# Performance work log

Hardware: AMD Instinct MI355X
Metric: run time of the kernel (lower is better)

Reference implementation:

```python
import jax, jax.numpy as jnp
import numpy as np

EPS = 1e-5

def setup_inputs() -> dict:
    key = jax.random.key(0)
    ks = jax.random.split(key, 16)
    B, C, H, W, HID = 32, 512, 56, 56, 128
    inp = {
        "x": jax.random.normal(ks[0], (B, C, H, W), jnp.float32),
        "mod": jax.random.randint(ks[1], (B,), 0, 2, jnp.int32),
        "w1_rgb": jax.random.normal(ks[2], (HID, C), jnp.float32) * 0.05,
        "rm_rgb": jax.random.normal(ks[3], (HID,), jnp.float32) * 0.1,
        "rv_rgb": jax.random.uniform(ks[4], (HID,), jnp.float32, 0.5, 1.5),
        "g_rgb": jax.random.uniform(ks[5], (HID,), jnp.float32, 0.5, 1.5),
        "b_rgb": jax.random.normal(ks[6], (HID,), jnp.float32) * 0.1,
        "w2_rgb": jax.random.normal(ks[7], (C, HID), jnp.float32) * 0.05,
        "w1_inf": jax.random.normal(ks[8], (HID, C), jnp.float32) * 0.05,
        "rm_inf": jax.random.normal(ks[9], (HID,), jnp.float32) * 0.1,
        "rv_inf": jax.random.uniform(ks[10], (HID,), jnp.float32, 0.5, 1.5),
        "g_inf": jax.random.uniform(ks[11], (HID,), jnp.float32, 0.5, 1.5),
        "b_inf": jax.random.normal(ks[12], (HID,), jnp.float32) * 0.1,
        "w2_inf": jax.random.normal(ks[13], (C, HID), jnp.float32) * 0.05,
    }
    return inp

def _branch(x, w1, rm, rv, g, b, w2):
    # 1x1 conv (no bias) -> BN (inference, running stats) -> ReLU -> 1x1 conv
    h = jnp.einsum('bchw,oc->bohw', x, w1)              # (B,HID,H,W)
    scale = g / jnp.sqrt(rv + EPS)                       # (HID,)
    shift = b - rm * scale
    h = jax.nn.relu(h * scale[None, :, None, None] + shift[None, :, None, None])
    return jnp.einsum('bchw,oc->bohw', h, w2)            # (B,C,H,W)

def reference(x, mod, w1_rgb, rm_rgb, rv_rgb, g_rgb, b_rgb, w2_rgb,
              w1_inf, rm_inf, rv_inf, g_inf, b_inf, w2_inf):
    rgb = _branch(x, w1_rgb, rm_rgb, rv_rgb, g_rgb, b_rgb, w2_rgb)
    inf = _branch(x, w1_inf, rm_inf, rv_inf, g_inf, b_inf, w2_inf)
    is_rgb = (mod == 1)[:, None, None, None]
    out = jnp.where(is_rgb, rgb, inf)  # mod in {0,1}; dropout is identity (eval)
    return out
```

## Files before the change

### kernel.cpp

```cpp
#include <hip/hip_runtime.h>
#include <hip/hip_bf16.h>
#include <stdint.h>

#define B_   32
#define C_   512
#define HW_  3136
#define HID_ 128
#define PT   64
#define XP   72
#define HP   136
#define EPS_ 1e-5f

using frag8  = __attribute__((ext_vector_type(8))) short;
using short8 = __attribute__((ext_vector_type(8))) short;
using f32x4  = __attribute__((ext_vector_type(4))) float;

__device__ __forceinline__ short f2bf(float f) {
    union { float f; uint32_t u; } v; v.f = f;
    uint32_t u = v.u;
    u += 0x7fffu + ((u >> 16) & 1u);
    return (short)(u >> 16);
}

__global__ __launch_bounds__(256) void prep_kernel(
    const float* __restrict__ w1_rgb, const float* __restrict__ w2_rgb,
    const float* __restrict__ w1_inf, const float* __restrict__ w2_inf,
    const float* __restrict__ rm_rgb, const float* __restrict__ rv_rgb,
    const float* __restrict__ g_rgb,  const float* __restrict__ b_rgb,
    const float* __restrict__ rm_inf, const float* __restrict__ rv_inf,
    const float* __restrict__ g_inf,  const float* __restrict__ b_inf,
    short* __restrict__ w1p_rgb, short* __restrict__ w1p_inf,
    short* __restrict__ w2p_rgb, short* __restrict__ w2p_inf,
    float* __restrict__ ss)
{
    int t = blockIdx.x * 256 + threadIdx.x;
    int p = t >> 9, w = t & 511;
    int q = w >> 7, r = (w >> 3) & 15, j = w & 7;
    {
        int mt = p >> 4, kt = p & 15;
        int m = mt * 16 + r, k = kt * 32 + q * 8 + j;
        w1p_rgb[t] = f2bf(w1_rgb[m * C_ + k]);
        w1p_inf[t] = f2bf(w1_inf[m * C_ + k]);
    }
    {
        int mt = p >> 2, kt = p & 3;
        int m = mt * 16 + r, k = kt * 32 + q * 8 + j;
        w2p_rgb[t] = f2bf(w2_rgb[m * HID_ + k]);
        w2p_inf[t] = f2bf(w2_inf[m * HID_ + k]);
    }
    if (t < 128) {
        float sc = g_rgb[t] * rsqrtf(rv_rgb[t] + EPS_);
        ss[t] = sc; ss[128 + t] = b_rgb[t] - rm_rgb[t] * sc;
    } else if (t < 256) {
        int i = t - 128;
        float sc = g_inf[i] * rsqrtf(rv_inf[i] + EPS_);
        ss[256 + i] = sc; ss[384 + i] = b_inf[i] - rm_inf[i] * sc;
    }
}

__global__ __launch_bounds__(256) void fused_kernel(
    const float* __restrict__ x, const int* __restrict__ mod,
    const short* __restrict__ w1p_rgb, const short* __restrict__ w1p_inf,
    const short* __restrict__ w2p_rgb, const short* __restrict__ w2p_inf,
    const float* __restrict__ ss, float* __restrict__ out)
{
    __shared__ short xlds[2][PT * XP];
    __shared__ short hlds[PT * HP];

    const int tid  = threadIdx.x;
    const int lane = tid & 63;
    const int wave = tid >> 6;
    const int i16  = lane & 15;
    const int q    = lane >> 4;
    const int b    = blockIdx.y;
    const int p0   = blockIdx.x * PT;

    const int is_rgb = (mod[b] == 1);
    const short* __restrict__ w1p = is_rgb ? w1p_rgb : w1p_inf;
    const short* __restrict__ w2p = is_rgb ? w2p_rgb : w2p_inf;
    const float* __restrict__ scale = ss + (is_rgb ? 0 : 256);
    const float* __restrict__ shift = scale + 128;

    f32x4 acc1[2][4];
    #pragma unroll
    for (int mt = 0; mt < 2; ++mt)
        #pragma unroll
        for (int nt = 0; nt < 4; ++nt)
            acc1[mt][nt] = (f32x4){0.f, 0.f, 0.f, 0.f};

    const int px    = lane;
    const int cbase = wave * 8;
    const float* __restrict__ xb = x + (size_t)b * C_ * HW_ + p0 + px;

    float rA[16], rB[16];
    #pragma unroll
    for (int it = 0; it < 2; ++it)
        #pragma unroll
        for (int j = 0; j < 8; ++j)
            rA[it * 8 + j] = xb[(size_t)(cbase + it * 32 + j) * HW_];

    #pragma unroll 1
    for (int k2 = 0; k2 < 4; ++k2) {
        const int kcA = k2 * 2, kcB = kcA + 1;

        #pragma unroll
        for (int it = 0; it < 2; ++it) {
            short8 pk;
            #pragma unroll
            for (int j = 0; j < 8; ++j) pk[j] = f2bf(rA[it * 8 + j]);
            *(short8*)(&xlds[0][px * XP + cbase + it * 32]) = pk;
        }
        __syncthreads();

        #pragma unroll
        for (int it = 0; it < 2; ++it)
            #pragma unroll
            for (int j = 0; j < 8; ++j)
                rB[it * 8 + j] = xb[(size_t)(kcB * 64 + cbase + it * 32 + j) * HW_];

        {
            frag8 af[2][2];
            #pragma unroll
            for (int kk = 0; kk < 2; ++kk) {
                int kt = kcA * 2 + kk;
                #pragma unroll
                for (int mt = 0; mt < 2; ++mt)
                    af[kk][mt] = *(const frag8*)(w1p + (((wave * 2 + mt) * 16 + kt) << 9) + lane * 8);
            }
            #pragma unroll
            for (int kk = 0; kk < 2; ++kk) {
                frag8 bfr[4];
                #pragma unroll
                for (int nt = 0; nt < 4; ++nt)
                    bfr[nt] = *(const frag8*)(&xlds[0][(nt * 16 + i16) * XP + kk * 32 + q * 8]);
                #pragma unroll
                for (int mt = 0; mt < 2; ++mt)
                    #pragma unroll
                    for (int nt = 0; nt < 4; ++nt)
                        acc1[mt][nt] = __builtin_amdgcn_mfma_f32_16x16x32_bf16(
                            af[kk][mt], bfr[nt], acc1[mt][nt], 0, 0, 0);
            }
        }

        #pragma unroll
        for (int it = 0; it < 2; ++it) {
            short8 pk;
            #pragma unroll
            for (int j = 0; j < 8; ++j) pk[j] = f2bf(rB[it * 8 + j]);
            *(short8*)(&xlds[1][px * XP + cbase + it * 32]) = pk;
        }
        __syncthreads();

        if (k2 < 3) {
            #pragma unroll
            for (int it = 0; it < 2; ++it)
                #pragma unroll
                for (int j = 0; j < 8; ++j)
                    rA[it * 8 + j] = xb[(size_t)((kcA + 2) * 64 + cbase + it * 32 + j) * HW_];
        }

        {
            frag8 af[2][2];
            #pragma unroll
            for (int kk = 0; kk < 2; ++kk) {
                int kt = kcB * 2 + kk;
                #pragma unroll
                for (int mt = 0; mt < 2; ++mt)
                    af[kk][mt] = *(const frag8*)(w1p + (((wave * 2 + mt) * 16 + kt) << 9) + lane * 8);
            }
            #pragma unroll
            for (int kk = 0; kk < 2; ++kk) {
                frag8 bfr[4];
                #pragma unroll
                for (int nt = 0; nt < 4; ++nt)
                    bfr[nt] = *(const frag8*)(&xlds[1][(nt * 16 + i16) * XP + kk * 32 + q * 8]);
                #pragma unroll
                for (int mt = 0; mt < 2; ++mt)
                    #pragma unroll
                    for (int nt = 0; nt < 4; ++nt)
                        acc1[mt][nt] = __builtin_amdgcn_mfma_f32_16x16x32_bf16(
                            af[kk][mt], bfr[nt], acc1[mt][nt], 0, 0, 0);
            }
        }
    }

    #pragma unroll
    for (int mt = 0; mt < 2; ++mt) {
        int mbase = wave * 32 + mt * 16 + q * 4;
        float s0 = scale[mbase + 0], s1 = scale[mbase + 1];
        float s2 = scale[mbase + 2], s3 = scale[mbase + 3];
        float h0 = shift[mbase + 0], h1 = shift[mbase + 1];
        float h2 = shift[mbase + 2], h3 = shift[mbase + 3];
        #pragma unroll
        for (int nt = 0; nt < 4; ++nt) {
            int p = nt * 16 + i16;
            short4 pk = make_short4(
                f2bf(fmaxf(acc1[mt][nt][0] * s0 + h0, 0.f)),
                f2bf(fmaxf(acc1[mt][nt][1] * s1 + h1, 0.f)),
                f2bf(fmaxf(acc1[mt][nt][2] * s2 + h2, 0.f)),
                f2bf(fmaxf(acc1[mt][nt][3] * s3 + h3, 0.f)));
            *(short4*)(&hlds[p * HP + mbase]) = pk;
        }
    }
    __syncthreads();

    #pragma unroll 1
    for (int half = 0; half < 2; ++half) {
        f32x4 acc2[4][4];
        #pragma unroll
        for (int pt = 0; pt < 4; ++pt)
            #pragma unroll
            for (int ct = 0; ct < 4; ++ct)
                acc2[pt][ct] = (f32x4){0.f, 0.f, 0.f, 0.f};

        #pragma unroll
        for (int kt = 0; kt < 4; ++kt) {
            frag8 wf[4];
            #pragma unroll
            for (int ct = 0; ct < 4; ++ct) {
                int ctg = half * 16 + wave * 4 + ct;
                wf[ct] = *(const frag8*)(w2p + ((ctg * 4 + kt) << 9) + lane * 8);
            }
            frag8 hf[4];
            #pragma unroll
            for (int pt = 0; pt < 4; ++pt)
                hf[pt] = *(const frag8*)(&hlds[(pt * 16 + i16) * HP + kt * 32 + q * 8]);
            #pragma unroll
            for (int pt = 0; pt < 4; ++pt)
                #pragma unroll
                for (int ct = 0; ct < 4; ++ct)
                    acc2[pt][ct] = __builtin_amdgcn_mfma_f32_16x16x32_bf16(
                        hf[pt], wf[ct], acc2[pt][ct], 0, 0, 0);
        }
        #pragma unroll
        for (int ct = 0; ct < 4; ++ct) {
            int crow = (half * 16 + wave * 4 + ct) * 16 + i16;
            float* obase = out + ((size_t)(b * C_ + crow)) * HW_ + p0 + q * 4;
            #pragma unroll
            for (int pt = 0; pt < 4; ++pt)
                __builtin_nontemporal_store(acc2[pt][ct], (f32x4*)(obase + pt * 16));
        }
    }
}

extern "C" void kernel_launch(void* const* d_in, const int* in_sizes, int n_in,
                              void* d_out, int out_size, void* d_ws, size_t ws_size,
                              hipStream_t stream) {
    const float* x      = (const float*)d_in[0];
    const int*   mod    = (const int*)d_in[1];
    const float* w1_rgb = (const float*)d_in[2];
    const float* rm_rgb = (const float*)d_in[3];
    const float* rv_rgb = (const float*)d_in[4];
    const float* g_rgb  = (const float*)d_in[5];
    const float* b_rgb  = (const float*)d_in[6];
    const float* w2_rgb = (const float*)d_in[7];
    const float* w1_inf = (const float*)d_in[8];
    const float* rm_inf = (const float*)d_in[9];
    const float* rv_inf = (const float*)d_in[10];
    const float* g_inf  = (const float*)d_in[11];
    const float* b_inf  = (const float*)d_in[12];
    const float* w2_inf = (const float*)d_in[13];
    float* out = (float*)d_out;

    char* ws = (char*)d_ws;
    short* w1p_rgb = (short*)(ws + 0);
    short* w1p_inf = (short*)(ws + 131072);
    short* w2p_rgb = (short*)(ws + 262144);
    short* w2p_inf = (short*)(ws + 393216);
    float* ss      = (float*)(ws + 524288);

    prep_kernel<<<256, 256, 0, stream>>>(
        w1_rgb, w2_rgb, w1_inf, w2_inf,
        rm_rgb, rv_rgb, g_rgb, b_rgb,
        rm_inf, rv_inf, g_inf, b_inf,
        w1p_rgb, w1p_inf, w2p_rgb, w2p_inf, ss);

    dim3 grid(HW_ / PT, B_);
    fused_kernel<<<grid, 256, 0, stream>>>(
        x, mod, w1p_rgb, w1p_inf, w2p_rgb, w2p_inf, ss, out);
}
```

Before: 419.4 us.

## Deepen x prefetch to two chunks ahead with triple register buffering

The first GEMM's K loop over 512 channels is fully unrolled into 8 chunks with a triple-buffered register array. Global loads for chunk c+2 are issued while chunk c is converted and multiplied, so two chunks are in flight instead of one. This is meant to hide more global-memory latency on the strided x reads, at the cost of more VGPRs and possibly lower occupancy. The output stores also change from nontemporal to ordinary stores.

```diff
diff --git a/kernel.cpp b/kernel.cpp
--- a/kernel.cpp
+++ b/kernel.cpp
@@ -92,95 +92,58 @@
     const int cbase = wave * 8;
     const float* __restrict__ xb = x + (size_t)b * C_ * HW_ + p0 + px;
 
-    float rA[16], rB[16];
-    #pragma unroll
-    for (int it = 0; it < 2; ++it)
-        #pragma unroll
-        for (int j = 0; j < 8; ++j)
-            rA[it * 8 + j] = xb[(size_t)(cbase + it * 32 + j) * HW_];
-
-    #pragma unroll 1
-    for (int k2 = 0; k2 < 4; ++k2) {
-        const int kcA = k2 * 2, kcB = kcA + 1;
+    float r[3][16];
+    #pragma unroll
+    for (int c0 = 0; c0 < 2; ++c0)
+        #pragma unroll
+        for (int it = 0; it < 2; ++it)
+            #pragma unroll
+            for (int j = 0; j < 8; ++j)
+                r[c0][it * 8 + j] =
+                    xb[(size_t)(c0 * 64 + cbase + it * 32 + j) * HW_];
+
+    #pragma unroll
+    for (int c = 0; c < 8; ++c) {
+        const int rb = c % 3, lb = c & 1;
 
         #pragma unroll
         for (int it = 0; it < 2; ++it) {
             short8 pk;
             #pragma unroll
-            for (int j = 0; j < 8; ++j) pk[j] = f2bf(rA[it * 8 + j]);
-            *(short8*)(&xlds[0][px * XP + cbase + it * 32]) = pk;
+            for (int j = 0; j < 8; ++j) pk[j] = f2bf(r[rb][it * 8 + j]);
+            *(short8*)(&xlds[lb][px * XP + cbase + it * 32]) = pk;
         }
         __syncthreads();
 
-        #pragma unroll
-        for (int it = 0; it < 2; ++it)
-            #pragma unroll
-            for (int j = 0; j < 8; ++j)
-                rB[it * 8 + j] = xb[(size_t)(kcB * 64 + cbase + it * 32 + j) * HW_];
-
-        {
-            frag8 af[2][2];
-            #pragma unroll
-            for (int kk = 0; kk < 2; ++kk) {
-                int kt = kcA * 2 + kk;
-                #pragma unroll
-                for (int mt = 0; mt < 2; ++mt)
-                    af[kk][mt] = *(const frag8*)(w1p + (((wave * 2 + mt) * 16 + kt) << 9) + lane * 8);
-            }
-            #pragma unroll
-            for (int kk = 0; kk < 2; ++kk) {
-                frag8 bfr[4];
-                #pragma unroll
-                for (int nt = 0; nt < 4; ++nt)
-                    bfr[nt] = *(const frag8*)(&xlds[0][(nt * 16 + i16) * XP + kk * 32 + q * 8]);
-                #pragma unroll
-                for (int mt = 0; mt < 2; ++mt)
-                    #pragma unroll
-                    for (int nt = 0; nt < 4; ++nt)
-                        acc1[mt][nt] = __builtin_amdgcn_mfma_f32_16x16x32_bf16(
-                            af[kk][mt], bfr[nt], acc1[mt][nt], 0, 0, 0);
-            }
-        }
-
-        #pragma unroll
-        for (int it = 0; it < 2; ++it) {
-            short8 pk;
-            #pragma unroll
-            for (int j = 0; j < 8; ++j) pk[j] = f2bf(rB[it * 8 + j]);
-            *(short8*)(&xlds[1][px * XP + cbase + it * 32]) = pk;
-        }
-        __syncthreads();
-
-        if (k2 < 3) {
+        if (c + 2 < 8) {
             #pragma unroll
             for (int it = 0; it < 2; ++it)
                 #pragma unroll
                 for (int j = 0; j < 8; ++j)
-                    rA[it * 8 + j] = xb[(size_t)((kcA + 2) * 64 + cbase + it * 32 + j) * HW_];
-        }
-
-        {
-            frag8 af[2][2];
-            #pragma unroll
-            for (int kk = 0; kk < 2; ++kk) {
-                int kt = kcB * 2 + kk;
-                #pragma unroll
-                for (int mt = 0; mt < 2; ++mt)
-                    af[kk][mt] = *(const frag8*)(w1p + (((wave * 2 + mt) * 16 + kt) << 9) + lane * 8);
-            }
-            #pragma unroll
-            for (int kk = 0; kk < 2; ++kk) {
-                frag8 bfr[4];
+                    r[(c + 2) % 3][it * 8 + j] =
+                        xb[(size_t)((c + 2) * 64 + cbase + it * 32 + j) * HW_];
+        }
+
+        frag8 af[2][2];
+        #pragma unroll
+        for (int kk = 0; kk < 2; ++kk) {
+            int kt = c * 2 + kk;
+            #pragma unroll
+            for (int mt = 0; mt < 2; ++mt)
+                af[kk][mt] = *(const frag8*)(w1p + (((wave * 2 + mt) * 16 + kt) << 9) + lane * 8);
+        }
+        #pragma unroll
+        for (int kk = 0; kk < 2; ++kk) {
+            frag8 bfr[4];
+            #pragma unroll
+            for (int nt = 0; nt < 4; ++nt)
+                bfr[nt] = *(const frag8*)(&xlds[lb][(nt * 16 + i16) * XP + kk * 32 + q * 8]);
+            #pragma unroll
+            for (int mt = 0; mt < 2; ++mt)
                 #pragma unroll
                 for (int nt = 0; nt < 4; ++nt)
-                    bfr[nt] = *(const frag8*)(&xlds[1][(nt * 16 + i16) * XP + kk * 32 + q * 8]);
-                #pragma unroll
-                for (int mt = 0; mt < 2; ++mt)
-                    #pragma unroll
-                    for (int nt = 0; nt < 4; ++nt)
-                        acc1[mt][nt] = __builtin_amdgcn_mfma_f32_16x16x32_bf16(
-                            af[kk][mt], bfr[nt], acc1[mt][nt], 0, 0, 0);
-            }
+                    acc1[mt][nt] = __builtin_amdgcn_mfma_f32_16x16x32_bf16(
+                        af[kk][mt], bfr[nt], acc1[mt][nt], 0, 0, 0);
         }
     }
 
@@ -238,7 +201,7 @@
             float* obase = out + ((size_t)(b * C_ + crow)) * HW_ + p0 + q * 4;
             #pragma unroll
             for (int pt = 0; pt < 4; ++pt)
-                __builtin_nontemporal_store(acc2[pt][ct], (f32x4*)(obase + pt * 16));
+                *(f32x4*)(obase + pt * 16) = acc2[pt][ct];
         }
     }
 }
```

Result: faster. 394.7 us (-5.9%).
